# Kernel optimization log

Hardware: AMD Instinct MI355X
Metric: run time of the kernel (lower is better)

The kernel has to match this reference:

```python
import jax, jax.numpy as jnp
import numpy as np

C = 1.0          # ball curvature magnitude (manifold.c)
EPS = 1e-5       # boundary projection epsilon
MIN_NORM = 1e-15

def _norm(x):
    return jnp.maximum(jnp.linalg.norm(x, axis=-1, keepdims=True), MIN_NORM)

def artanh(x):
    return jnp.arctanh(jnp.clip(x, -1.0 + 1e-7, 1.0 - 1e-7))

def proj(x, c=C):
    # clip points to the open Poincare ball of radius 1/sqrt(c)
    n = _norm(x)
    maxnorm = (1.0 - EPS) / jnp.sqrt(c)
    return jnp.where(n > maxnorm, x / n * maxnorm, x)

def logmap0(x, c=C):
    sc = jnp.sqrt(c)
    n = _norm(x)
    return artanh(sc * n) * x / (sc * n)

def expmap0(u, c=C):
    sc = jnp.sqrt(c)
    n = _norm(u)
    return jnp.tanh(sc * n) * u / (sc * n)

def gyro_add(x, y, c=C):
    # Mobius (gyrovector) addition
    x2 = jnp.sum(x * x, -1, keepdims=True)
    y2 = jnp.sum(y * y, -1, keepdims=True)
    xy = jnp.sum(x * y, -1, keepdims=True)
    num = (1.0 + 2.0 * c * xy + c * y2) * x + (1.0 - c * x2) * y
    den = 1.0 + 2.0 * c * xy + c * c * x2 * y2
    return num / jnp.maximum(den, MIN_NORM)

def gyro_matvec(W, x, c=C):
    # Mobius matrix-vector multiplication (pv_gyro_matvec)
    sc = jnp.sqrt(c)
    xn = _norm(x)
    mx = x @ W.T                       # [N, out]
    mxn = _norm(mx)
    res = jnp.tanh(mxn / xn * artanh(sc * xn)) * mx / (mxn * sc)
    zero = jnp.all(mx == 0.0, axis=-1, keepdims=True)
    return jnp.where(zero, jnp.zeros_like(res), res)

def hyp_linear(x, W, b, c=C):
    # CustomHyperbolicLinear (activation=None branch): mobius matvec + hyp bias gyro-add
    res = proj(gyro_matvec(W, x, c), c)
    hyp_bias = proj(expmap0(b[None, :], c), c)   # proj_tan0 is identity on the ball
    res = proj(gyro_add(res, hyp_bias, c), c)
    return res

def hyp_tanh_act(x, c=C):
    # CustomHyperbolicActivation(manifold, nn.Tanh()): tanh in tangent space at origin
    x = proj(x, c)
    t = jnp.tanh(logmap0(x, c))
    return proj(expmap0(t, c), c)


def setup_inputs() -> dict:
    key = jax.random.key(0)
    k0, k1, k2 = jax.random.split(key, 3)
    N, D, H = 32768, 1024, 1024
    x = proj(0.1 * jax.random.normal(k0, (N, D), dtype=jnp.float32))
    gain = float(np.sqrt(2.0))
    bound1 = gain * float(np.sqrt(6.0 / (D + H)))   # xavier_uniform with gain sqrt(2)
    W1 = jax.random.uniform(k1, (H, D), jnp.float32, -bound1, bound1)
    b1 = jnp.zeros((H,), jnp.float32)
    bound2 = gain * float(np.sqrt(6.0 / (H + H)))
    W2 = jax.random.uniform(k2, (H, H), jnp.float32, -bound2, bound2)
    b2 = jnp.zeros((H,), jnp.float32)
    return {"x": x, "W1": W1, "b1": b1, "W2": W2, "b2": b2}


def reference(x, W1, b1, W2, b2):
    # GeometricModel forward: two CustomHyperbolicLayer blocks
    # (hyperbolic linear -> tangent-space tanh activation)
    h = hyp_linear(x, W1, b1)
    h = hyp_tanh_act(h)
    h = hyp_linear(h, W2, b2)
    h = hyp_tanh_act(h)
    return h
```

## Files before the change

kernel.cpp:

```cpp
#include <hip/hip_runtime.h>


typedef short short8 __attribute__((ext_vector_type(8)));
typedef unsigned short u16x8 __attribute__((ext_vector_type(8)));
typedef unsigned short u16x4 __attribute__((ext_vector_type(4)));
typedef float f32x4 __attribute__((ext_vector_type(4)));

#define MAXN (1.0f - 1e-5f)

__device__ __forceinline__ float bf2f(unsigned short u) {
    return __uint_as_float(((unsigned int)u) << 16);
}
__device__ __forceinline__ unsigned short f2bf(float f) {
    unsigned int u = __float_as_uint(f);
    u += 0x7FFFu + ((u >> 16) & 1u);
    return (unsigned short)(u >> 16);
}
__device__ __forceinline__ float wave_sum(float v) {
#pragma unroll
    for (int m = 32; m > 0; m >>= 1) v += __shfl_xor(v, m, 64);
    return v;
}
__device__ __forceinline__ float artanh_clip(float x) {
    x = fminf(fmaxf(x, -1.0f + 1e-7f), 1.0f - 1e-7f);
    return 0.5f * logf((1.0f + x) / (1.0f - x));
}

__device__ __forceinline__ void gld_lds16(const unsigned short* g, unsigned short* l) {
    __builtin_amdgcn_global_load_lds(
        (const __attribute__((address_space(1))) unsigned int*)g,
        (__attribute__((address_space(3))) unsigned int*)l,
        16, 0, 0);
}

__global__ __launch_bounds__(256) void cast_x_kernel(
    const float* __restrict__ X, unsigned short* __restrict__ Xb,
    float* __restrict__ xn, int K)
{
    int row = blockIdx.x * 4 + (threadIdx.x >> 6);
    int l = threadIdx.x & 63;
    const float4* xr = (const float4*)(X + (size_t)row * K);
    u16x4* xw = (u16x4*)(Xb + (size_t)row * K);
    float ss = 0.f;
#pragma unroll
    for (int i = 0; i < 4; ++i) {
        float4 v = xr[i * 64 + l];
        ss += v.x * v.x + v.y * v.y + v.z * v.z + v.w * v.w;
        u16x4 o;
        o[0] = f2bf(v.x); o[1] = f2bf(v.y); o[2] = f2bf(v.z); o[3] = f2bf(v.w);
        xw[i * 64 + l] = o;
    }
    ss = wave_sum(ss);
    if (l == 0) xn[row] = fmaxf(sqrtf(ss), 1e-15f);
}

__global__ __launch_bounds__(256) void cast_w_kernel(
    const float* __restrict__ W1, unsigned short* __restrict__ W1b,
    const float* __restrict__ W2, unsigned short* __restrict__ W2b, int n4each)
{
    int i = blockIdx.x * 256 + threadIdx.x;
    const float4* src;
    u16x4* dst;
    if (i < n4each) { src = (const float4*)W1; dst = (u16x4*)W1b; }
    else            { src = (const float4*)W2; dst = (u16x4*)W2b; i -= n4each; }
    float4 v = src[i];
    u16x4 o;
    o[0] = f2bf(v.x); o[1] = f2bf(v.y); o[2] = f2bf(v.z); o[3] = f2bf(v.w);
    dst[i] = o;
}

#define STAGE(rs_, kt_) do {                                            \
    const int ko_ = (kt_) << 5;                                         \
    gld_lds16(Ab + ga0 + ko_, &sA[(rs_) * 8192 + c0 * 8]);              \
    gld_lds16(Ab + ga1 + ko_, &sA[(rs_) * 8192 + c1 * 8]);              \
    gld_lds16(Bb + ga0 + ko_, &sB[(rs_) * 8192 + c0 * 8]);              \
    gld_lds16(Bb + ga1 + ko_, &sB[(rs_) * 8192 + c1 * 8]);              \
} while (0)

#define LDFRAG(FA_, FB_, kt_) do {                                                  \
    const int rb_ = ((kt_) & 3) * 8192;                                             \
    const unsigned short* pa_ = &sA[rb_ + (wm + lr) * 32 + swo];                    \
    const unsigned short* pb_ = &sB[rb_ + (wn + lr) * 32 + swo];                    \
    _Pragma("unroll")                                                               \
    for (int m_ = 0; m_ < 8; ++m_) FA_[m_] = *(const short8*)(pa_ + m_ * 512);      \
    _Pragma("unroll")                                                               \
    for (int n_ = 0; n_ < 4; ++n_) FB_[n_] = *(const short8*)(pb_ + n_ * 512);      \
} while (0)

#define MFMAB(FA_, FB_)                                                             \
    _Pragma("unroll")                                                               \
    for (int m_ = 0; m_ < 8; ++m_)                                                  \
        _Pragma("unroll")                                                           \
        for (int n_ = 0; n_ < 4; ++n_)                                              \
            acc[m_][n_] = __builtin_amdgcn_mfma_f32_16x16x32_bf16(                  \
                FA_[m_], FB_[n_], acc[m_][n_], 0, 0, 0);

#define PSTEP(kt_, FAC_, FBC_, FAN_, FBN_, DOSTAGE_, DOPF_, DOVM_, VMSTR_, DOBAR_) {\
    if (DOSTAGE_) { STAGE((((kt_) + 3) & 3), (kt_) + 3); }                          \
    if (DOPF_) { LDFRAG(FAN_, FBN_, (kt_) + 1); }                                   \
    __builtin_amdgcn_s_setprio(1);                                                  \
    MFMAB(FAC_, FBC_);                                                              \
    __builtin_amdgcn_s_setprio(0);                                                  \
    if (DOVM_) { asm volatile("s_waitcnt vmcnt(" VMSTR_ ")" ::: "memory"); }        \
    if (DOBAR_) { __builtin_amdgcn_s_barrier(); }                                   \
}

__global__ __launch_bounds__(512, 2) void gemm_bt_kernel(
    const unsigned short* __restrict__ A,
    const unsigned short* __restrict__ B,
    unsigned short* __restrict__ C,
    int M, int Nc, int K)
{
    __shared__ __align__(16) unsigned short sA[4 * 256 * 32];
    __shared__ __align__(16) unsigned short sB[4 * 256 * 32];

    const int t = threadIdx.x;
    const int l = t & 63;
    const int w = t >> 6;
    const int lr = l & 15;
    const int lq = l >> 4;

    const int nwg = gridDim.x;
    const int cpx = nwg >> 3;
    const int swz = (blockIdx.x & 7) * cpx + (blockIdx.x >> 3);
    const int nb = Nc >> 8;
    const int bm = swz / nb;
    const int bn = swz % nb;

    const unsigned short* Ab = A + (size_t)bm * 256 * K;
    const unsigned short* Bb = B + (size_t)bn * 256 * K;

    const int wm = (w >> 2) * 128;
    const int wn = (w & 3) * 64;

    const int c0 = t, c1 = t + 512;
    const int r0 = c0 >> 2, s0 = (c0 & 3) ^ ((r0 >> 1) & 3);
    const int r1 = c1 >> 2, s1 = (c1 & 3) ^ ((r1 >> 1) & 3);
    const size_t ga0 = (size_t)r0 * K + s0 * 8;
    const size_t ga1 = (size_t)r1 * K + s1 * 8;

    const int swo = (lq ^ ((lr >> 1) & 3)) * 8;

    f32x4 acc[8][4];
#pragma unroll
    for (int i = 0; i < 8; ++i)
#pragma unroll
        for (int j = 0; j < 4; ++j)
            acc[i][j] = (f32x4){0.f, 0.f, 0.f, 0.f};

    STAGE(0, 0);
    STAGE(1, 1);
    STAGE(2, 2);
    asm volatile("s_waitcnt vmcnt(4)" ::: "memory");
    __builtin_amdgcn_s_barrier();

    short8 fa0[8], fb0[4], fa1[8], fb1[4];
    LDFRAG(fa0, fb0, 0);

    const int NTK = K >> 5;
    int kt = 0;
#pragma unroll 1
    for (; kt < NTK - 4; kt += 2) {
        PSTEP(kt,     fa0, fb0, fa1, fb1, true, true, true, "4", true);
        PSTEP(kt + 1, fa1, fb1, fa0, fb0, true, true, true, "4", true);
    }
    PSTEP(NTK - 4, fa0, fb0, fa1, fb1, true,  true,  true,  "4", true);
    PSTEP(NTK - 3, fa1, fb1, fa0, fb0, false, true,  true,  "0", true);
    PSTEP(NTK - 2, fa0, fb0, fa1, fb1, false, true,  false, "0", false);
    PSTEP(NTK - 1, fa1, fb1, fa0, fb0, false, false, false, "0", false);

    unsigned short* Cb = C + (size_t)(bm * 256 + wm) * Nc + bn * 256 + wn;
#pragma unroll
    for (int i = 0; i < 8; ++i)
#pragma unroll
        for (int r = 0; r < 4; ++r) {
            unsigned short* Cr = Cb + (size_t)(i * 16 + lq * 4 + r) * Nc + lr;
#pragma unroll
            for (int j = 0; j < 4; ++j)
                Cr[j * 16] = f2bf(acc[i][j][r]);
        }
}

template <int OUTF32>
__global__ __launch_bounds__(256) void hyp_epilogue_kernel(
    const unsigned short* __restrict__ mx, const float* __restrict__ xn_in,
    const float* __restrict__ bvec, void* __restrict__ outp,
    float* __restrict__ xn_out, int H)
{
    int row = blockIdx.x * 4 + (threadIdx.x >> 6);
    int l = threadIdx.x & 63;
    const u16x8* mrow = (const u16x8*)(mx + (size_t)row * H);
    u16x8 mv0 = mrow[l], mv1 = mrow[64 + l];
    const float4* bf4 = (const float4*)bvec;
    float4 bq0 = bf4[l * 2], bq1 = bf4[l * 2 + 1];
    float4 bq2 = bf4[128 + l * 2], bq3 = bf4[128 + l * 2 + 1];

    float m[16], b[16];
#pragma unroll
    for (int i = 0; i < 8; ++i) { m[i] = bf2f(mv0[i]); m[8 + i] = bf2f(mv1[i]); }
    b[0] = bq0.x; b[1] = bq0.y; b[2] = bq0.z; b[3] = bq0.w;
    b[4] = bq1.x; b[5] = bq1.y; b[6] = bq1.z; b[7] = bq1.w;
    b[8] = bq2.x; b[9] = bq2.y; b[10] = bq2.z; b[11] = bq2.w;
    b[12] = bq3.x; b[13] = bq3.y; b[14] = bq3.z; b[15] = bq3.w;

    float ssm = 0.f, ssb = 0.f, dmb = 0.f;
#pragma unroll
    for (int i = 0; i < 16; ++i) {
        ssm += m[i] * m[i]; ssb += b[i] * b[i]; dmb += m[i] * b[i];
    }
    ssm = wave_sum(ssm); ssb = wave_sum(ssb); dmb = wave_sum(dmb);

    float mxn = fmaxf(sqrtf(ssm), 1e-15f);
    float bn  = fmaxf(sqrtf(ssb), 1e-15f);
    float xn  = xn_in[row];

    float tt = tanhf(mxn / xn * artanh_clip(xn));
    float rnorm = fabsf(tt);
    float pr = (rnorm > MAXN) ? (MAXN / rnorm) : 1.0f;
    float resScale = tt * pr / mxn;
    float rn = fminf(rnorm, MAXN);
    float x2 = rn * rn;

    float tb = tanhf(bn);
    float hbn = fabsf(tb);
    float pb = (hbn > MAXN) ? (MAXN / hbn) : 1.0f;
    float hscale = (tb / bn) * pb;
    float hn = fminf(hbn, MAXN);
    float y2 = hn * hn;

    float xy = resScale * hscale * dmb;
    float ca = 1.0f + 2.0f * xy + y2;
    float cb = 1.0f - x2;
    float den = fmaxf(1.0f + 2.0f * xy + x2 * y2, 1e-15f);
    float fA = ca * resScale / den;
    float fB = cb * hscale / den;

    float ssz = fA * fA * ssm + 2.0f * fA * fB * dmb + fB * fB * ssb;
    float zn = fmaxf(sqrtf(fmaxf(ssz, 0.0f)), 1e-15f);
    float pz = (zn > MAXN) ? (MAXN / zn) : 1.0f;
    float n2 = fmaxf(fminf(zn, MAXN), 1e-15f);
    float g = (artanh_clip(n2) / n2) * pz;

    float u[16];
    float ssu = 0.f;
#pragma unroll
    for (int i = 0; i < 16; ++i) {
        float zi = fA * m[i] + fB * b[i];
        u[i] = tanhf(g * zi);
        ssu += u[i] * u[i];
    }
    ssu = wave_sum(ssu);
    float un = fmaxf(sqrtf(ssu), 1e-15f);
    float te = tanhf(un);
    float on = fabsf(te);
    float po = (on > MAXN) ? (MAXN / on) : 1.0f;
    float os = (te / un) * po;

    if (OUTF32) {
        float* of = (float*)outp + (size_t)row * H;
        float4* of4 = (float4*)of;
        float4 a0, a1, a2, a3;
        a0.x = os * u[0];  a0.y = os * u[1];  a0.z = os * u[2];  a0.w = os * u[3];
        a1.x = os * u[4];  a1.y = os * u[5];  a1.z = os * u[6];  a1.w = os * u[7];
        a2.x = os * u[8];  a2.y = os * u[9];  a2.z = os * u[10]; a2.w = os * u[11];
        a3.x = os * u[12]; a3.y = os * u[13]; a3.z = os * u[14]; a3.w = os * u[15];
        of4[l * 2] = a0; of4[l * 2 + 1] = a1;
        of4[128 + l * 2] = a2; of4[128 + l * 2 + 1] = a3;
    } else {
        u16x8 o0, o1;
#pragma unroll
        for (int i = 0; i < 8; ++i) { o0[i] = f2bf(os * u[i]); o1[i] = f2bf(os * u[8 + i]); }
        u16x8* orow = (u16x8*)((unsigned short*)outp + (size_t)row * H);
        orow[l] = o0; orow[64 + l] = o1;
    }
    if (l == 0) xn_out[row] = fmaxf(fminf(on, MAXN), 1e-15f);
}

extern "C" void kernel_launch(void* const* d_in, const int* in_sizes, int n_in,
                              void* d_out, int out_size, void* d_ws, size_t ws_size,
                              hipStream_t stream)
{
    const float* x  = (const float*)d_in[0];
    const float* W1 = (const float*)d_in[1];
    const float* b1 = (const float*)d_in[2];
    const float* W2 = (const float*)d_in[3];
    const float* b2 = (const float*)d_in[4];

    const int H = in_sizes[2];
    const int D = in_sizes[1] / H;
    const int N = in_sizes[0] / D;

    unsigned short* stage = (unsigned short*)d_out;
    float* outf = (float*)d_out;

    unsigned short* mxb = (unsigned short*)d_ws;
    unsigned short* W1b = mxb + (size_t)N * H;
    unsigned short* W2b = W1b + (size_t)H * D;
    float* xn1 = (float*)(W2b + (size_t)H * H);
    float* xn2 = xn1 + N;

    dim3 blk(256);
    dim3 gblk(512);
    const int gemm_grid = (N / 256) * (H / 256);
    const int n4w = H * D / 4;

    cast_x_kernel<<<N / 4, blk, 0, stream>>>(x, stage, xn1, D);
    cast_w_kernel<<<(2 * n4w + 255) / 256, blk, 0, stream>>>(W1, W1b, W2, W2b, n4w);
    gemm_bt_kernel<<<gemm_grid, gblk, 0, stream>>>(stage, W1b, mxb, N, H, D);
    hyp_epilogue_kernel<0><<<N / 4, blk, 0, stream>>>(mxb, xn1, b1, stage, xn2, H);
    gemm_bt_kernel<<<gemm_grid, gblk, 0, stream>>>(stage, W2b, mxb, N, H, H);
    hyp_epilogue_kernel<1><<<N / 4, blk, 0, stream>>>(mxb, xn2, b2, outf, xn1, H);
}
```

Before: 457.0 us.

## Restructure GEMM main loop into 8-phase ping-pong schedule with 64-wide K tiles

Replaces the 4-stage 32-wide K pipeline with a double-buffered 64-wide K tile and an eight-phase schedule per iteration. Each phase reads one quadrant of fragments, issues half-tile global-to-LDS loads for the next tile, and runs one quadrant of MFMAs, with a new 8-slot XOR swizzle. The aim is to interleave LDS reads, global loads and MFMA work more finely, hiding memory latency behind compute. It adds two barriers per phase and depends on exact vmcnt accounting, which risks stalls or subtle hazards.

```diff
diff --git a/kernel.cpp b/kernel.cpp
--- a/kernel.cpp
+++ b/kernel.cpp
@@ -69,40 +69,60 @@
     dst[i] = o;
 }
 
-#define STAGE(rs_, kt_) do {                                            \
-    const int ko_ = (kt_) << 5;                                         \
-    gld_lds16(Ab + ga0 + ko_, &sA[(rs_) * 8192 + c0 * 8]);              \
-    gld_lds16(Ab + ga1 + ko_, &sA[(rs_) * 8192 + c1 * 8]);              \
-    gld_lds16(Bb + ga0 + ko_, &sB[(rs_) * 8192 + c0 * 8]);              \
-    gld_lds16(Bb + ga1 + ko_, &sB[(rs_) * 8192 + c1 * 8]);              \
+
+#define VMC(n_) asm volatile("s_waitcnt vmcnt(" #n_ ")" ::: "memory")
+
+#define STAGE_A(half_, kt_) do {                                                    \
+    unsigned short* ld_ = (unsigned short*)sA +                                     \
+        (((kt_) & 1) * 16384 + (half_) * 8192 + t * 8);                             \
+    const size_t go_ = (size_t)((half_) * 128) * K + (size_t)(kt_) * 64 + gr0;      \
+    gld_lds16(Ab + go_, ld_);                                                       \
+    gld_lds16(Ab + go_ + (size_t)64 * K, ld_ + 4096);                               \
 } while (0)
 
-#define LDFRAG(FA_, FB_, kt_) do {                                                  \
-    const int rb_ = ((kt_) & 3) * 8192;                                             \
-    const unsigned short* pa_ = &sA[rb_ + (wm + lr) * 32 + swo];                    \
-    const unsigned short* pb_ = &sB[rb_ + (wn + lr) * 32 + swo];                    \
-    _Pragma("unroll")                                                               \
-    for (int m_ = 0; m_ < 8; ++m_) FA_[m_] = *(const short8*)(pa_ + m_ * 512);      \
-    _Pragma("unroll")                                                               \
-    for (int n_ = 0; n_ < 4; ++n_) FB_[n_] = *(const short8*)(pb_ + n_ * 512);      \
+#define STAGE_B(half_, kt_) do {                                                    \
+    unsigned short* ld_ = (unsigned short*)sB +                                     \
+        (((kt_) & 1) * 16384 + (half_) * 8192 + t * 8);                             \
+    const size_t go_ = (size_t)((half_) * 128) * K + (size_t)(kt_) * 64 + gr0;      \
+    gld_lds16(Bb + go_, ld_);                                                       \
+    gld_lds16(Bb + go_ + (size_t)64 * K, ld_ + 4096);                               \
 } while (0)
 
-#define MFMAB(FA_, FB_)                                                             \
-    _Pragma("unroll")                                                               \
-    for (int m_ = 0; m_ < 8; ++m_)                                                  \
-        _Pragma("unroll")                                                           \
-        for (int n_ = 0; n_ < 4; ++n_)                                              \
-            acc[m_][n_] = __builtin_amdgcn_mfma_f32_16x16x32_bf16(                  \
-                FA_[m_], FB_[n_], acc[m_][n_], 0, 0, 0);
-
-#define PSTEP(kt_, FAC_, FBC_, FAN_, FBN_, DOSTAGE_, DOPF_, DOVM_, VMSTR_, DOBAR_) {\
-    if (DOSTAGE_) { STAGE((((kt_) + 3) & 3), (kt_) + 3); }                          \
-    if (DOPF_) { LDFRAG(FAN_, FBN_, (kt_) + 1); }                                   \
+#define RD_A4(lo_, db_)                                                             \
+    _Pragma("unroll")                                                               \
+    for (int mm_ = 0; mm_ < 4; ++mm_) {                                             \
+        a[(lo_) + mm_][0] = *(const short8*)&sA[(db_) + ah + ((lo_) + mm_) * 1024 + swp];        \
+        a[(lo_) + mm_][1] = *(const short8*)&sA[(db_) + ah + ((lo_) + mm_) * 1024 + (swp ^ 32)]; \
+    }
+
+#define RD_B2(lo_, db_)                                                             \
+    _Pragma("unroll")                                                               \
+    for (int nn_ = 0; nn_ < 2; ++nn_) {                                             \
+        b[(lo_) + nn_][0] = *(const short8*)&sB[(db_) + bh + ((lo_) + nn_) * 1024 + swp];        \
+        b[(lo_) + nn_][1] = *(const short8*)&sB[(db_) + bh + ((lo_) + nn_) * 1024 + (swp ^ 32)]; \
+    }
+
+#define MF_Q(M0_, N0_)                                                              \
+    _Pragma("unroll")                                                               \
+    for (int kk_ = 0; kk_ < 2; ++kk_)                                               \
+    _Pragma("unroll")                                                               \
+    for (int mm_ = 0; mm_ < 4; ++mm_)                                               \
+    _Pragma("unroll")                                                               \
+    for (int nn_ = 0; nn_ < 2; ++nn_)                                               \
+        acc[(M0_) + mm_][(N0_) + nn_] = __builtin_amdgcn_mfma_f32_16x16x32_bf16(    \
+            a[(M0_) + mm_][kk_], b[(N0_) + nn_][kk_],                               \
+            acc[(M0_) + mm_][(N0_) + nn_], 0, 0, 0);
+
+#define PH(RD_, ST_, VM_, MQ_) {                                                    \
+    RD_;                                                                            \
+    ST_;                                                                            \
+    __builtin_amdgcn_s_barrier();                                                   \
+    asm volatile("s_waitcnt lgkmcnt(0)" ::: "memory");                              \
     __builtin_amdgcn_s_setprio(1);                                                  \
-    MFMAB(FAC_, FBC_);                                                              \
+    MQ_;                                                                            \
     __builtin_amdgcn_s_setprio(0);                                                  \
-    if (DOVM_) { asm volatile("s_waitcnt vmcnt(" VMSTR_ ")" ::: "memory"); }        \
-    if (DOBAR_) { __builtin_amdgcn_s_barrier(); }                                   \
+    VM_;                                                                            \
+    __builtin_amdgcn_s_barrier();                                                   \
 }
 
 __global__ __launch_bounds__(512, 2) void gemm_bt_kernel(
@@ -111,8 +131,8 @@
     unsigned short* __restrict__ C,
     int M, int Nc, int K)
 {
-    __shared__ __align__(16) unsigned short sA[4 * 256 * 32];
-    __shared__ __align__(16) unsigned short sB[4 * 256 * 32];
+    __shared__ __align__(16) unsigned short sA[2 * 256 * 64];
+    __shared__ __align__(16) unsigned short sB[2 * 256 * 64];
 
     const int t = threadIdx.x;
     const int l = t & 63;
@@ -133,13 +153,13 @@
     const int wm = (w >> 2) * 128;
     const int wn = (w & 3) * 64;
 
-    const int c0 = t, c1 = t + 512;
-    const int r0 = c0 >> 2, s0 = (c0 & 3) ^ ((r0 >> 1) & 3);
-    const int r1 = c1 >> 2, s1 = (c1 & 3) ^ ((r1 >> 1) & 3);
-    const size_t ga0 = (size_t)r0 * K + s0 * 8;
-    const size_t ga1 = (size_t)r1 * K + s1 * 8;
-
-    const int swo = (lq ^ ((lr >> 1) & 3)) * 8;
+    const int grow = t >> 3;
+    const int gslot = ((t & 7) ^ (grow & 7)) * 8;
+    const size_t gr0 = (size_t)grow * K + gslot;
+
+    const int ah = (wm >> 7) * 8192 + lr * 64;
+    const int bh = (wn >> 7) * 8192 + (wn & 64) * 64 + lr * 64;
+    const int swp = (lq ^ (lr & 7)) * 8;
 
     f32x4 acc[8][4];
 #pragma unroll
@@ -148,26 +168,39 @@
         for (int j = 0; j < 4; ++j)
             acc[i][j] = (f32x4){0.f, 0.f, 0.f, 0.f};
 
-    STAGE(0, 0);
-    STAGE(1, 1);
-    STAGE(2, 2);
-    asm volatile("s_waitcnt vmcnt(4)" ::: "memory");
+    short8 a[8][2], b[4][2];
+
+    STAGE_A(0, 0); STAGE_A(1, 0); STAGE_B(0, 0); STAGE_B(1, 0);
+    STAGE_A(0, 1); STAGE_A(1, 1);
+    VMC(4);
     __builtin_amdgcn_s_barrier();
 
-    short8 fa0[8], fb0[4], fa1[8], fb1[4];
-    LDFRAG(fa0, fb0, 0);
-
-    const int NTK = K >> 5;
-    int kt = 0;
+    const int NTK = K >> 6;
+    const int NI = NTK >> 1;
+
 #pragma unroll 1
-    for (; kt < NTK - 4; kt += 2) {
-        PSTEP(kt,     fa0, fb0, fa1, fb1, true, true, true, "4", true);
-        PSTEP(kt + 1, fa1, fb1, fa0, fb0, true, true, true, "4", true);
-    }
-    PSTEP(NTK - 4, fa0, fb0, fa1, fb1, true,  true,  true,  "4", true);
-    PSTEP(NTK - 3, fa1, fb1, fa0, fb0, false, true,  true,  "0", true);
-    PSTEP(NTK - 2, fa0, fb0, fa1, fb1, false, true,  false, "0", false);
-    PSTEP(NTK - 1, fa1, fb1, fa0, fb0, false, false, false, "0", false);
+    for (int it = 0; it < NI - 1; ++it) {
+        const int T = it * 2;
+        PH(RD_A4(0, 0); RD_B2(0, 0),         STAGE_B(0, T + 1), (void)0, MF_Q(0, 0));
+        PH(RD_A4(4, 0),                      STAGE_B(1, T + 1), (void)0, MF_Q(4, 0));
+        PH(RD_B2(2, 0),                      STAGE_A(0, T + 2), (void)0, MF_Q(4, 2));
+        PH((void)0,                          STAGE_A(1, T + 2), VMC(4),  MF_Q(0, 2));
+        PH(RD_A4(0, 16384); RD_B2(0, 16384), STAGE_B(0, T + 2), (void)0, MF_Q(0, 0));
+        PH(RD_A4(4, 16384),                  STAGE_B(1, T + 2), (void)0, MF_Q(4, 0));
+        PH(RD_B2(2, 16384),                  STAGE_A(0, T + 3), (void)0, MF_Q(4, 2));
+        PH((void)0,                          STAGE_A(1, T + 3), VMC(4),  MF_Q(0, 2));
+    }
+    {
+        const int T = NTK - 2;
+        PH(RD_A4(0, 0); RD_B2(0, 0),         STAGE_B(0, T + 1), (void)0, MF_Q(0, 0));
+        PH(RD_A4(4, 0),                      STAGE_B(1, T + 1), (void)0, MF_Q(4, 0));
+        PH(RD_B2(2, 0),                      (void)0,           (void)0, MF_Q(4, 2));
+        PH((void)0,                          (void)0,           VMC(0),  MF_Q(0, 2));
+        PH(RD_A4(0, 16384); RD_B2(0, 16384), (void)0,           (void)0, MF_Q(0, 0));
+        PH(RD_A4(4, 16384),                  (void)0,           (void)0, MF_Q(4, 0));
+        PH(RD_B2(2, 16384),                  (void)0,           (void)0, MF_Q(4, 2));
+        PH((void)0,                          (void)0,           (void)0, MF_Q(0, 2));
+    }
 
     unsigned short* Cb = C + (size_t)(bm * 256 + wm) * Nc + bn * 256 + wn;
 #pragma unroll
```

Measured after the change: 478.1 us. 4.6% more time.
